# Kernel tuning notes

Measured on AMD Instinct MI355X. Metric: run time of the kernel, lower is better.

Reference implementation:

```python
import jax, jax.numpy as jnp
import numpy as np

B, T, C, H, RANK = 4, 2048, 1024, 16, 8


def _lora_linear(x, W, b, A, Bm):
    # loralib-style: y = x W^T + b + (x A^T) B^T  (scaling alpha/r = 1)
    return x @ W.T + b + (x @ A.T) @ Bm.T


def setup_inputs() -> dict:
    key = jax.random.key(0)
    ks = jax.random.split(key, 6)
    s_in = 1.0 / np.sqrt(C)
    return {
        "x": jax.random.normal(ks[0], (B, T, C), jnp.float32),
        "c_attn_w": jax.random.normal(ks[1], (3 * C, C), jnp.float32) * s_in,
        "c_attn_b": jnp.zeros((3 * C,), jnp.float32),
        "c_attn_A": jax.random.normal(ks[2], (RANK, C), jnp.float32) * s_in,
        "c_attn_B": jnp.zeros((3 * C, RANK), jnp.float32),
        "c_proj_w": jax.random.normal(ks[3], (C, C), jnp.float32) * s_in,
        "c_proj_b": jnp.zeros((C,), jnp.float32),
        "c_proj_A": jax.random.normal(ks[4], (RANK, C), jnp.float32) * s_in,
        "c_proj_B": jnp.zeros((C, RANK), jnp.float32),
        "n_head": H,
    }


def reference(x, c_attn_w, c_attn_b, c_attn_A, c_attn_B,
              c_proj_w, c_proj_b, c_proj_A, c_proj_B, n_head):
    Bsz, Tlen, Cd = x.shape
    d = Cd // n_head
    qkv = _lora_linear(x, c_attn_w, c_attn_b, c_attn_A, c_attn_B)  # [B,T,3C]
    q, k, v = jnp.split(qkv, 3, axis=2)
    query, key_out = q, k  # returned pre-reshape, as in torch
    # [B, H, T, d]
    qh = q.reshape(Bsz, Tlen, n_head, d).transpose(0, 2, 1, 3)
    kh = k.reshape(Bsz, Tlen, n_head, d).transpose(0, 2, 1, 3)
    vh = v.reshape(Bsz, Tlen, n_head, d).transpose(0, 2, 1, 3)
    att = jnp.einsum('bhqd,bhkd->bhqk', qh, kh) * (1.0 / np.sqrt(d))
    causal = jnp.tril(jnp.ones((Tlen, Tlen), bool))
    att = jnp.where(causal[None, None], att, -jnp.inf)
    att = jax.nn.softmax(att, axis=-1)
    y = jnp.einsum('bhqk,bhkd->bhqd', att, vh)
    y = y.transpose(0, 2, 1, 3).reshape(Bsz, Tlen, Cd)
    out = _lora_linear(y, c_proj_w, c_proj_b, c_proj_A, c_proj_B)
    return out, query, key_out
```

## Files before the change

### kernel.cpp

```cpp
#include <hip/hip_runtime.h>
#include <stdint.h>

#define T_LEN 2048
#define C_DIM 1024
#define NHEAD 16
#define DHEAD 64
#define QOFF  8388608L
#define KOFF  16777216L
#define SCALE_LOG2 0.18033688011112042f

typedef float f32x4 __attribute__((ext_vector_type(4)));
typedef short bf16x8 __attribute__((ext_vector_type(8)));
typedef short s16x4 __attribute__((ext_vector_type(4)));
typedef unsigned short u16;

__device__ __forceinline__ float b2f(u16 h) {
  union { uint32_t u; float f; } v; v.u = ((uint32_t)h) << 16; return v.f;
}
__device__ __forceinline__ u16 f2b(float f) {
  union { float f; uint32_t u; } v; v.f = f;
  uint32_t r = v.u + 0x7fffu + ((v.u >> 16) & 1u);
  return (u16)(r >> 16);
}
__device__ __forceinline__ u16 f2b_tr(float f) {
  union { float f; uint32_t u; } v; v.f = f;
  return (u16)(v.u >> 16);
}
__device__ __forceinline__ void async16(const u16* g, u16* l) {
  __builtin_amdgcn_global_load_lds((const __attribute__((address_space(1))) void*)g,
                                   (__attribute__((address_space(3))) void*)l, 16, 0, 0);
}

#define MFMA16 __builtin_amdgcn_mfma_f32_16x16x32_bf16

__global__ __launch_bounds__(256) void prep_all(const float* __restrict__ x,
                                                u16* __restrict__ xc,
                                                const float* __restrict__ w1,
                                                const float* __restrict__ B1,
                                                const float* __restrict__ A1,
                                                u16* __restrict__ w1e,
                                                const float* __restrict__ w2,
                                                const float* __restrict__ B2,
                                                const float* __restrict__ A2,
                                                u16* __restrict__ w2e) {
  int b = blockIdx.x;
  if (b < 8192) {
    long i = ((long)b * 256 + threadIdx.x) * 4;
    f32x4 v = *(const f32x4*)(x + i);
    s16x4 r;
    r[0] = (short)f2b(v[0]); r[1] = (short)f2b(v[1]);
    r[2] = (short)f2b(v[2]); r[3] = (short)f2b(v[3]);
    *(s16x4*)(xc + i) = r;
  } else if (b < 20480) {
    int i = (b - 8192) * 256 + threadIdx.x;
    int n = i >> 10, k = i & 1023;
    float acc = w1[i];
#pragma unroll
    for (int r = 0; r < 8; r++) acc += B1[n * 8 + r] * A1[r * 1024 + k];
    w1e[i] = f2b(acc);
  } else {
    int i = (b - 20480) * 256 + threadIdx.x;
    int n = i >> 10, k = i & 1023;
    float acc = w2[i];
#pragma unroll
    for (int r = 0; r < 8; r++) acc += B2[n * 8 + r] * A2[r * 1024 + k];
    w2e[i] = f2b(acc);
  }
}

template <int MODE>
__global__ __launch_bounds__(256) void gemm_bt(const u16* __restrict__ A,
                                               const u16* __restrict__ Bt,
                                               const float* __restrict__ bias,
                                               float* __restrict__ outf,
                                               u16* __restrict__ kc,
                                               u16* __restrict__ vblk, int K) {
  __shared__ __align__(16) u16 ldsA[128 * 32];
  __shared__ __align__(16) u16 ldsB[128 * 32];
  const int t = threadIdx.x;
  const int lane = t & 63, l15 = lane & 15, quad = lane >> 4, w = t >> 6;
  const int wr = (w >> 1) * 64, wc = (w & 1) * 64;
  const long rowA = (long)blockIdx.y * 128;
  const long rowB = (long)blockIdx.x * 128;
  const int srow = t >> 2, scol = (t & 3) * 8;

  f32x4 acc[4][4];
#pragma unroll
  for (int i = 0; i < 4; i++)
#pragma unroll
    for (int j = 0; j < 4; j++) { f32x4 z = {0.f, 0.f, 0.f, 0.f}; acc[i][j] = z; }

  const u16* Ab = A + rowA * K;
  const u16* Bb = Bt + rowB * K;
  for (int k0 = 0; k0 < K; k0 += 32) {
    __syncthreads();
    async16(Ab + (long)srow * K + k0 + scol, &ldsA[t * 8]);
    async16(Ab + (long)(srow + 64) * K + k0 + scol, &ldsA[2048 + t * 8]);
    async16(Bb + (long)srow * K + k0 + scol, &ldsB[t * 8]);
    async16(Bb + (long)(srow + 64) * K + k0 + scol, &ldsB[2048 + t * 8]);
    __syncthreads();
    bf16x8 af[4], bfr[4];
#pragma unroll
    for (int g = 0; g < 4; g++) {
      af[g]  = *(const bf16x8*)&ldsA[(wr + g * 16 + l15) * 32 + quad * 8];
      bfr[g] = *(const bf16x8*)&ldsB[(wc + g * 16 + l15) * 32 + quad * 8];
    }
#pragma unroll
    for (int i = 0; i < 4; i++)
#pragma unroll
      for (int j = 0; j < 4; j++)
        acc[i][j] = MFMA16(af[i], bfr[j], acc[i][j], 0, 0, 0);
  }

#pragma unroll
  for (int i = 0; i < 4; i++) {
#pragma unroll
    for (int j = 0; j < 4; j++) {
      int n = (int)rowB + wc + j * 16 + l15;
      float bv = bias[n];
#pragma unroll
      for (int r = 0; r < 4; r++) {
        int m = (int)rowA + wr + i * 16 + quad * 4 + r;
        float val = acc[i][j][r] + bv;
        if constexpr (MODE == 1) {
          outf[(long)m * C_DIM + n] = val;
        } else {
          int sec = n >> 10;
          int nc = n & 1023;
          int h = nc >> 6, dd = nc & 63;
          int bb = m >> 11, tt = m & 2047;
          int bh = bb * NHEAD + h;
          if (sec == 0) {
            outf[QOFF + (long)m * C_DIM + nc] = val;
          } else if (sec == 1) {
            outf[KOFF + (long)m * C_DIM + nc] = val;
            kc[(long)bh * (T_LEN * 64) + (long)tt * 64 + dd] = f2b(val);
          } else {
            vblk[(long)bh * (T_LEN * 64) + (long)(tt >> 6) * 4096 + dd * 64 + (tt & 63)] = f2b(val);
          }
        }
      }
    }
  }
}

__global__ __launch_bounds__(256) void flash_attn(const float* __restrict__ qsec,
                                                  const u16* __restrict__ kc,
                                                  const u16* __restrict__ vblk,
                                                  u16* __restrict__ yb) {
  __shared__ __align__(16) u16 ldsK[64 * 64];
  __shared__ __align__(16) u16 ldsV[64 * 64];
  __shared__ __align__(16) u16 plds[4][32 * 72];
  const int t = threadIdx.x;
  const int lane = t & 63, l15 = lane & 15, quad = lane >> 4, w = t >> 6;
  const int p = blockIdx.x >> 6;
  const int bh = blockIdx.x & 63;
  const int bb = bh >> 4, h = bh & 15;

  bf16x8 ones;
#pragma unroll
  for (int j = 0; j < 8; j++) ones[j] = (short)0x3F80;

  const u16* kcb = kc + (long)bh * (T_LEN * 64);
  const u16* vbb = vblk + (long)bh * (T_LEN * 64);
  const int l0 = t, l1 = 256 + t;
  const int s0c = ((l0 >> 3) * 8 + ((l0 & 7) ^ ((l0 >> 3) & 7))) * 8;
  const int s1c = ((l1 >> 3) * 8 + ((l1 & 7) ^ ((l1 >> 3) & 7))) * 8;

#pragma unroll 1
  for (int half = 0; half < 2; half++) {
    const int qt = half ? p : (15 - p);
    const int q0 = qt * 128;

    const float* Qb = qsec + ((long)bb * T_LEN + q0 + w * 32) * C_DIM + h * DHEAD;
    bf16x8 qf[2][2];
#pragma unroll
    for (int rg = 0; rg < 2; rg++)
#pragma unroll
      for (int kk = 0; kk < 2; kk++) {
        const float* ptr = Qb + (long)(rg * 16 + l15) * C_DIM + kk * 32 + quad * 8;
        f32x4 a = *(const f32x4*)ptr, b = *(const f32x4*)(ptr + 4);
        bf16x8 r;
        r[0] = (short)f2b(a[0] * SCALE_LOG2); r[1] = (short)f2b(a[1] * SCALE_LOG2);
        r[2] = (short)f2b(a[2] * SCALE_LOG2); r[3] = (short)f2b(a[3] * SCALE_LOG2);
        r[4] = (short)f2b(b[0] * SCALE_LOG2); r[5] = (short)f2b(b[1] * SCALE_LOG2);
        r[6] = (short)f2b(b[2] * SCALE_LOG2); r[7] = (short)f2b(b[3] * SCALE_LOG2);
        qf[rg][kk] = r;
      }

    f32x4 o[2][4];
    f32x4 ls[2];
#pragma unroll
    for (int rg = 0; rg < 2; rg++) {
#pragma unroll
      for (int cg = 0; cg < 4; cg++) { f32x4 z = {0.f, 0.f, 0.f, 0.f}; o[rg][cg] = z; }
      f32x4 z = {0.f, 0.f, 0.f, 0.f}; ls[rg] = z;
    }

    const int qminw = q0 + w * 32;
    const int nkt = (q0 + 128) >> 6;
    for (int kt = 0; kt < nkt; kt++) {
      const int kb0 = kt * 64;
      __syncthreads();
      {
        const u16* ks = kcb + (long)kb0 * 64;
        const u16* vs = vbb + (long)kt * 4096;
        async16(ks + s0c, &ldsK[l0 * 8]);
        async16(ks + s1c, &ldsK[l1 * 8]);
        async16(vs + s0c, &ldsV[l0 * 8]);
        async16(vs + s1c, &ldsV[l1 * 8]);
      }
      __syncthreads();
      if (kb0 > qminw + 31) continue;

      f32x4 s[2][4];
#pragma unroll
      for (int rg = 0; rg < 2; rg++)
#pragma unroll
        for (int kg = 0; kg < 4; kg++) { f32x4 z = {0.f, 0.f, 0.f, 0.f}; s[rg][kg] = z; }
#pragma unroll
      for (int kg = 0; kg < 4; kg++) {
        int row = kg * 16 + l15, sw = row & 7;
        bf16x8 kf0 = *(const bf16x8*)&ldsK[row * 64 + ((quad ^ sw) * 8)];
        bf16x8 kf1 = *(const bf16x8*)&ldsK[row * 64 + (((4 + quad) ^ sw) * 8)];
#pragma unroll
        for (int rg = 0; rg < 2; rg++) {
          s[rg][kg] = MFMA16(qf[rg][0], kf0, s[rg][kg], 0, 0, 0);
          s[rg][kg] = MFMA16(qf[rg][1], kf1, s[rg][kg], 0, 0, 0);
        }
      }
      const bool needMask = (kb0 + 63) > qminw;
#pragma unroll
      for (int rg = 0; rg < 2; rg++) {
#pragma unroll
        for (int r = 0; r < 4; r++) {
          float v0 = s[rg][0][r], v1 = s[rg][1][r], v2 = s[rg][2][r], v3 = s[rg][3][r];
          if (needMask) {
            int qrow = qminw + rg * 16 + quad * 4 + r;
            if (kb0 + l15 > qrow)      v0 = -3.0e38f;
            if (kb0 + 16 + l15 > qrow) v1 = -3.0e38f;
            if (kb0 + 32 + l15 > qrow) v2 = -3.0e38f;
            if (kb0 + 48 + l15 > qrow) v3 = -3.0e38f;
          }
          int prow = rg * 16 + quad * 4 + r;
          plds[w][prow * 72 + l15]      = f2b_tr(exp2f(v0));
          plds[w][prow * 72 + 16 + l15] = f2b_tr(exp2f(v1));
          plds[w][prow * 72 + 32 + l15] = f2b_tr(exp2f(v2));
          plds[w][prow * 72 + 48 + l15] = f2b_tr(exp2f(v3));
        }
      }
      asm volatile("s_waitcnt lgkmcnt(0)" ::: "memory");
      bf16x8 pf[2][2];
#pragma unroll
      for (int rg = 0; rg < 2; rg++)
#pragma unroll
        for (int kk = 0; kk < 2; kk++)
          pf[rg][kk] = *(const bf16x8*)&plds[w][(rg * 16 + l15) * 72 + kk * 32 + quad * 8];
#pragma unroll
      for (int rg = 0; rg < 2; rg++) {
        ls[rg] = MFMA16(pf[rg][0], ones, ls[rg], 0, 0, 0);
        ls[rg] = MFMA16(pf[rg][1], ones, ls[rg], 0, 0, 0);
      }
#pragma unroll
      for (int cg = 0; cg < 4; cg++) {
        int row = cg * 16 + l15, sw = row & 7;
        bf16x8 vf0 = *(const bf16x8*)&ldsV[row * 64 + ((quad ^ sw) * 8)];
        bf16x8 vf1 = *(const bf16x8*)&ldsV[row * 64 + (((4 + quad) ^ sw) * 8)];
#pragma unroll
        for (int rg = 0; rg < 2; rg++) {
          o[rg][cg] = MFMA16(pf[rg][0], vf0, o[rg][cg], 0, 0, 0);
          o[rg][cg] = MFMA16(pf[rg][1], vf1, o[rg][cg], 0, 0, 0);
        }
      }
    }

#pragma unroll
    for (int rg = 0; rg < 2; rg++) {
#pragma unroll
      for (int r = 0; r < 4; r++) {
        float inv = 1.0f / ls[rg][r];
        int tt = q0 + w * 32 + rg * 16 + quad * 4 + r;
        long base = ((long)bb * T_LEN + tt) * C_DIM + h * DHEAD;
#pragma unroll
        for (int cg = 0; cg < 4; cg++)
          yb[base + cg * 16 + l15] = f2b(o[rg][cg][r] * inv);
      }
    }
  }
}

extern "C" void kernel_launch(void* const* d_in, const int* in_sizes, int n_in,
                              void* d_out, int out_size, void* d_ws, size_t ws_size,
                              hipStream_t stream) {
  const float* x  = (const float*)d_in[0];
  const float* w1 = (const float*)d_in[1];
  const float* b1 = (const float*)d_in[2];
  const float* A1 = (const float*)d_in[3];
  const float* B1 = (const float*)d_in[4];
  const float* w2 = (const float*)d_in[5];
  const float* b2 = (const float*)d_in[6];
  const float* A2 = (const float*)d_in[7];
  const float* B2 = (const float*)d_in[8];
  float* outf = (float*)d_out;
  u16* outb16 = (u16*)d_out;

  u16* ws  = (u16*)d_ws;
  u16* w2e = ws;
  u16* w1e = ws + 1048576;
  u16* xc  = ws + 4194304;
  u16* yb  = ws + 1048576;
  u16* vblk = outb16;
  u16* kcp  = outb16 + 8388608;

  prep_all<<<24576, 256, 0, stream>>>(x, xc, w1, B1, A1, w1e, w2, B2, A2, w2e);
  gemm_bt<0><<<dim3(24, 64), 256, 0, stream>>>(xc, w1e, b1, outf, kcp, vblk, 1024);
  flash_attn<<<512, 256, 0, stream>>>(outf + QOFF, kcp, vblk, yb);
  gemm_bt<1><<<dim3(8, 64), 256, 0, stream>>>(yb, w2e, b2, outf, nullptr, nullptr, 1024);
}
```

Before: 357.1 us.

## Fuse all stages into one cooperative persistent kernel with grid syncs

Replaces the four separate launches (prep, QKV GEMM, flash attention, output GEMM) with a single cooperative kernel of 512 blocks that loops over work units and uses grid.sync between stages. This removes launch gaps and inter-kernel idle tails. It also replaces the padded P scratch in LDS with an XOR-swizzled 64-wide layout. The price is a fixed 512-block grid and grid-wide barriers, which can cost occupancy and load balance (the QKV GEMM runs 3 tiles per block, and prep runs many small units). The old multi-kernel path is kept as a fallback.

```diff
diff --git a/kernel.cpp b/kernel.cpp
--- a/kernel.cpp
+++ b/kernel.cpp
@@ -1,5 +1,8 @@
 #include <hip/hip_runtime.h>
+#include <hip/hip_cooperative_groups.h>
 #include <stdint.h>
+
+namespace cg = cooperative_groups;
 
 #define T_LEN 2048
 #define C_DIM 1024
@@ -14,9 +17,6 @@
 typedef short s16x4 __attribute__((ext_vector_type(4)));
 typedef unsigned short u16;
 
-__device__ __forceinline__ float b2f(u16 h) {
-  union { uint32_t u; float f; } v; v.u = ((uint32_t)h) << 16; return v.f;
-}
 __device__ __forceinline__ u16 f2b(float f) {
   union { float f; uint32_t u; } v; v.f = f;
   uint32_t r = v.u + 0x7fffu + ((v.u >> 16) & 1u);
@@ -33,17 +33,16 @@
 
 #define MFMA16 __builtin_amdgcn_mfma_f32_16x16x32_bf16
 
-__global__ __launch_bounds__(256) void prep_all(const float* __restrict__ x,
-                                                u16* __restrict__ xc,
-                                                const float* __restrict__ w1,
-                                                const float* __restrict__ B1,
-                                                const float* __restrict__ A1,
-                                                u16* __restrict__ w1e,
-                                                const float* __restrict__ w2,
-                                                const float* __restrict__ B2,
-                                                const float* __restrict__ A2,
-                                                u16* __restrict__ w2e) {
-  int b = blockIdx.x;
+__device__ __forceinline__ void prep_unit(int b, const float* __restrict__ x,
+                                          u16* __restrict__ xc,
+                                          const float* __restrict__ w1,
+                                          const float* __restrict__ B1,
+                                          const float* __restrict__ A1,
+                                          u16* __restrict__ w1e,
+                                          const float* __restrict__ w2,
+                                          const float* __restrict__ B2,
+                                          const float* __restrict__ A2,
+                                          u16* __restrict__ w2e) {
   if (b < 8192) {
     long i = ((long)b * 256 + threadIdx.x) * 4;
     f32x4 v = *(const f32x4*)(x + i);
@@ -69,19 +68,22 @@
 }
 
 template <int MODE>
-__global__ __launch_bounds__(256) void gemm_bt(const u16* __restrict__ A,
-                                               const u16* __restrict__ Bt,
-                                               const float* __restrict__ bias,
-                                               float* __restrict__ outf,
-                                               u16* __restrict__ kc,
-                                               u16* __restrict__ vblk, int K) {
-  __shared__ __align__(16) u16 ldsA[128 * 32];
-  __shared__ __align__(16) u16 ldsB[128 * 32];
+__device__ __forceinline__ void gemm_tile(int bx, int by,
+                                          const u16* __restrict__ A,
+                                          const u16* __restrict__ Bt,
+                                          const float* __restrict__ bias,
+                                          float* __restrict__ outf,
+                                          u16* __restrict__ kc,
+                                          u16* __restrict__ vblk,
+                                          u16* lds) {
+  u16* ldsA = lds;
+  u16* ldsB = lds + 4096;
+  const int K = 1024;
   const int t = threadIdx.x;
   const int lane = t & 63, l15 = lane & 15, quad = lane >> 4, w = t >> 6;
   const int wr = (w >> 1) * 64, wc = (w & 1) * 64;
-  const long rowA = (long)blockIdx.y * 128;
-  const long rowB = (long)blockIdx.x * 128;
+  const long rowA = (long)by * 128;
+  const long rowB = (long)bx * 128;
   const int srow = t >> 2, scol = (t & 3) * 8;
 
   f32x4 acc[4][4];
@@ -144,17 +146,17 @@
   }
 }
 
-__global__ __launch_bounds__(256) void flash_attn(const float* __restrict__ qsec,
-                                                  const u16* __restrict__ kc,
-                                                  const u16* __restrict__ vblk,
-                                                  u16* __restrict__ yb) {
-  __shared__ __align__(16) u16 ldsK[64 * 64];
-  __shared__ __align__(16) u16 ldsV[64 * 64];
-  __shared__ __align__(16) u16 plds[4][32 * 72];
+__device__ __forceinline__ void flash_block_paired(int bid, const float* __restrict__ qsec,
+                                                   const u16* __restrict__ kc,
+                                                   const u16* __restrict__ vblk,
+                                                   u16* __restrict__ yb, u16* lds) {
+  u16* ldsK = lds;
+  u16* ldsV = lds + 4096;
   const int t = threadIdx.x;
   const int lane = t & 63, l15 = lane & 15, quad = lane >> 4, w = t >> 6;
-  const int p = blockIdx.x >> 6;
-  const int bh = blockIdx.x & 63;
+  u16* pldsw = lds + 8192 + w * 2048;
+  const int p = bid >> 6;
+  const int bh = bid & 63;
   const int bb = bh >> 4, h = bh & 15;
 
   bf16x8 ones;
@@ -243,10 +245,13 @@
             if (kb0 + 48 + l15 > qrow) v3 = -3.0e38f;
           }
           int prow = rg * 16 + quad * 4 + r;
-          plds[w][prow * 72 + l15]      = f2b_tr(exp2f(v0));
-          plds[w][prow * 72 + 16 + l15] = f2b_tr(exp2f(v1));
-          plds[w][prow * 72 + 32 + l15] = f2b_tr(exp2f(v2));
-          plds[w][prow * 72 + 48 + l15] = f2b_tr(exp2f(v3));
+          int sw8 = prow & 7;
+          int cb = l15 >> 3;
+          int rb = prow * 64 + (l15 & 7);
+          pldsw[rb + ((((0 + cb) ^ sw8)) << 3)] = f2b_tr(exp2f(v0));
+          pldsw[rb + ((((2 + cb) ^ sw8)) << 3)] = f2b_tr(exp2f(v1));
+          pldsw[rb + ((((4 + cb) ^ sw8)) << 3)] = f2b_tr(exp2f(v2));
+          pldsw[rb + ((((6 + cb) ^ sw8)) << 3)] = f2b_tr(exp2f(v3));
         }
       }
       asm volatile("s_waitcnt lgkmcnt(0)" ::: "memory");
@@ -255,7 +260,8 @@
       for (int rg = 0; rg < 2; rg++)
 #pragma unroll
         for (int kk = 0; kk < 2; kk++)
-          pf[rg][kk] = *(const bf16x8*)&plds[w][(rg * 16 + l15) * 72 + kk * 32 + quad * 8];
+          pf[rg][kk] = *(const bf16x8*)&pldsw[(rg * 16 + l15) * 64 +
+                                             (((kk * 4 + quad) ^ (l15 & 7)) << 3)];
 #pragma unroll
       for (int rg = 0; rg < 2; rg++) {
         ls[rg] = MFMA16(pf[rg][0], ones, ls[rg], 0, 0, 0);
@@ -287,6 +293,71 @@
       }
     }
   }
+}
+
+__global__ __launch_bounds__(256) void prep_all(const float* __restrict__ x,
+                                                u16* __restrict__ xc,
+                                                const float* __restrict__ w1,
+                                                const float* __restrict__ B1,
+                                                const float* __restrict__ A1,
+                                                u16* __restrict__ w1e,
+                                                const float* __restrict__ w2,
+                                                const float* __restrict__ B2,
+                                                const float* __restrict__ A2,
+                                                u16* __restrict__ w2e) {
+  prep_unit(blockIdx.x, x, xc, w1, B1, A1, w1e, w2, B2, A2, w2e);
+}
+
+template <int MODE>
+__global__ __launch_bounds__(256) void gemm_bt(const u16* __restrict__ A,
+                                               const u16* __restrict__ Bt,
+                                               const float* __restrict__ bias,
+                                               float* __restrict__ outf,
+                                               u16* __restrict__ kc,
+                                               u16* __restrict__ vblk) {
+  __shared__ __align__(16) u16 lds[8192];
+  gemm_tile<MODE>(blockIdx.x, blockIdx.y, A, Bt, bias, outf, kc, vblk, lds);
+}
+
+__global__ __launch_bounds__(256) void flash_attn(const float* __restrict__ qsec,
+                                                  const u16* __restrict__ kc,
+                                                  const u16* __restrict__ vblk,
+                                                  u16* __restrict__ yb) {
+  __shared__ __align__(16) u16 lds[16384];
+  flash_block_paired(blockIdx.x, qsec, kc, vblk, yb, lds);
+}
+
+__global__ __launch_bounds__(256, 2) void fused_all(
+    const float* __restrict__ x,
+    const float* __restrict__ w1, const float* __restrict__ b1,
+    const float* __restrict__ A1, const float* __restrict__ B1,
+    const float* __restrict__ w2, const float* __restrict__ b2,
+    const float* __restrict__ A2, const float* __restrict__ B2,
+    float* __restrict__ outf, u16* __restrict__ xc, u16* __restrict__ w1e,
+    u16* __restrict__ w2e, u16* __restrict__ yb, u16* __restrict__ kc,
+    u16* __restrict__ vblk) {
+  cg::grid_group grid = cg::this_grid();
+  __shared__ __align__(16) u16 lds[16384];
+  const int bid = blockIdx.x;
+
+  for (int u = bid; u < 24576; u += 512)
+    prep_unit(u, x, xc, w1, B1, A1, w1e, w2, B2, A2, w2e);
+  __threadfence();
+  grid.sync();
+
+#pragma unroll 1
+  for (int rpt = 0; rpt < 3; rpt++) {
+    int idx = bid + rpt * 512;
+    gemm_tile<0>(idx % 24, idx / 24, xc, w1e, b1, outf, kc, vblk, lds);
+  }
+  __threadfence();
+  grid.sync();
+
+  flash_block_paired(bid, outf + QOFF, kc, vblk, yb, lds);
+  __threadfence();
+  grid.sync();
+
+  gemm_tile<1>(bid & 7, bid >> 3, yb, w2e, b2, outf, nullptr, nullptr, lds);
 }
 
 extern "C" void kernel_launch(void* const* d_in, const int* in_sizes, int n_in,
@@ -312,8 +383,32 @@
   u16* vblk = outb16;
   u16* kcp  = outb16 + 8388608;
 
+  static int coop_ok = -1;
+  if (coop_ok < 0) {
+    int dev = 0;
+    hipGetDevice(&dev);
+    int attr = 0;
+    hipDeviceGetAttribute(&attr, hipDeviceAttributeCooperativeLaunch, dev);
+    int nb = 0;
+    hipOccupancyMaxActiveBlocksPerMultiprocessor(&nb, (const void*)fused_all, 256, 0);
+    coop_ok = (attr != 0 && nb >= 2) ? 1 : 0;
+  }
+
+  if (coop_ok == 1) {
+    void* args[] = {
+      (void*)&x, (void*)&w1, (void*)&b1, (void*)&A1, (void*)&B1,
+      (void*)&w2, (void*)&b2, (void*)&A2, (void*)&B2,
+      (void*)&outf, (void*)&xc, (void*)&w1e, (void*)&w2e, (void*)&yb,
+      (void*)&kcp, (void*)&vblk
+    };
+    hipError_t e = hipLaunchCooperativeKernel((const void*)fused_all, dim3(512),
+                                              dim3(256), args, 0, stream);
+    if (e == hipSuccess) return;
+    coop_ok = 0;
+  }
+
   prep_all<<<24576, 256, 0, stream>>>(x, xc, w1, B1, A1, w1e, w2, B2, A2, w2e);
-  gemm_bt<0><<<dim3(24, 64), 256, 0, stream>>>(xc, w1e, b1, outf, kcp, vblk, 1024);
+  gemm_bt<0><<<dim3(24, 64), 256, 0, stream>>>(xc, w1e, b1, outf, kcp, vblk);
   flash_attn<<<512, 256, 0, stream>>>(outf + QOFF, kcp, vblk, yb);
-  gemm_bt<1><<<dim3(8, 64), 256, 0, stream>>>(yb, w2e, b2, outf, nullptr, nullptr, 1024);
-}
+  gemm_bt<1><<<dim3(8, 64), 256, 0, stream>>>(yb, w2e, b2, outf, nullptr, nullptr);
+}
```

Result: no change. 357.3 us (+0.0%).
